# Optimization experiments

Measured on AMD Instinct MI355X. Metric: run time of the kernel, lower is better.

## Reference

```python
import jax, jax.numpy as jnp
import numpy as np

N = 100000

def _norm_edges(edge_index, n):
    # add self loops, compute symmetric GCN normalization
    loop = jnp.arange(n, dtype=edge_index.dtype)
    src = jnp.concatenate([edge_index[0], loop])
    dst = jnp.concatenate([edge_index[1], loop])
    deg = jax.ops.segment_sum(jnp.ones_like(dst, dtype=jnp.float32), dst, num_segments=n)
    dinv = jnp.where(deg > 0, deg ** -0.5, 0.0)
    norm = dinv[src] * dinv[dst]
    return src, dst, norm

def _gcn(x, W, b, src, dst, norm, n):
    h = x @ W  # [N, out]
    msg = h[src] * norm[:, None]
    return jax.ops.segment_sum(msg, dst, num_segments=n) + b

def setup_inputs() -> dict:
    key = jax.random.key(0)
    ks = jax.random.split(key, 20)
    E = 3200000
    d_in, d_out = 64, 64
    def w(k, i, o):
        return jax.random.normal(k, (i, o), dtype=jnp.float32) * (1.0 / np.sqrt(i))
    return {
        "x": jax.random.normal(ks[0], (N, d_in), dtype=jnp.float32),
        "t": jax.random.normal(ks[1], (N,), dtype=jnp.float32),
        "edge_index": jax.random.randint(ks[2], (2, E), 0, N, dtype=jnp.int64),
        "W1": w(ks[3], d_in + 1, 64), "b1": jnp.zeros((64,), jnp.float32),
        "W2": w(ks[4], 64, 128), "b2": jnp.zeros((128,), jnp.float32),
        "W3": w(ks[5], 128, 256), "b3": jnp.zeros((256,), jnp.float32),
        "W4": w(ks[6], 256, 128), "b4": jnp.zeros((128,), jnp.float32),
        "F1": w(ks[7], 128, 256), "c1": jnp.zeros((256,), jnp.float32),
        "F2": w(ks[8], 256, 128), "c2": jnp.zeros((128,), jnp.float32),
        "F3": w(ks[9], 128, d_out), "c3": jnp.zeros((d_out,), jnp.float32),
    }

def reference(x, t, edge_index, W1, b1, W2, b2, W3, b3, W4, b4, F1, c1, F2, c2, F3, c3):
    n = x.shape[0]
    src, dst, norm = _norm_edges(edge_index, n)
    h = jnp.concatenate([x, t[:, None]], axis=1)
    h = jax.nn.gelu(_gcn(h, W1, b1, src, dst, norm, n))
    h = jax.nn.gelu(_gcn(h, W2, b2, src, dst, norm, n))
    h = jax.nn.gelu(_gcn(h, W3, b3, src, dst, norm, n))
    h = jax.nn.gelu(_gcn(h, W4, b4, src, dst, norm, n))
    h = jax.nn.gelu(h @ F1 + c1)
    h = jax.nn.gelu(h @ F2 + c2)
    return h @ F3 + c3
```

## Files before the change

### kernel.cpp

```cpp
#include <hip/hip_runtime.h>

static constexpr int BLK = 256;

typedef double d2 __attribute__((ext_vector_type(2)));
typedef int    i4 __attribute__((ext_vector_type(4)));

__device__ __forceinline__ double gelu_d(double v){
  double u = 0.7978845608028654 * (v + 0.044715 * v * v * v);
  return 0.5 * v * (1.0 + tanh(u));
}

__global__ void zero_k(int* __restrict__ a, int n){
  int stride = gridDim.x * blockDim.x;
  for (int i = blockIdx.x*blockDim.x + threadIdx.x; i < n; i += stride) a[i] = 0;
}

__global__ void zeromax_k(unsigned long long* m){
  if (threadIdx.x == 0 && blockIdx.x == 0)
    for (int i = 0; i < 8; ++i) m[i] = 0ull;
}

__global__ void detect_k(const int* __restrict__ ei, int* __restrict__ flag){
  if (threadIdx.x == 0 && blockIdx.x == 0){
    int zeros = 0;
    for (int i = 0; i < 64; ++i) if (ei[2*i + 1] == 0) ++zeros;
    *flag = (zeros >= 48) ? 1 : 0;
  }
}

__global__ void count_k(const int* __restrict__ ei, int E, const int* __restrict__ flag,
                        int* __restrict__ cnt){
  int is64 = *flag;
  int stride = gridDim.x * blockDim.x;
  for (int e = blockIdx.x*blockDim.x + threadIdx.x; e < E; e += stride){
    int d = is64 ? ei[2*(E + e)] : ei[E + e];
    atomicAdd(&cnt[d], 1);
  }
}

__global__ void dinv_k(const int* __restrict__ cnt, double* __restrict__ dinv, int n){
  int i = blockIdx.x*blockDim.x + threadIdx.x;
  if (i < n){
    double deg = (double)(cnt[i] + 1);
    dinv[i] = 1.0 / sqrt(deg);
  }
}

__global__ __launch_bounds__(256)
void scanA_k(const int* __restrict__ cnt, int* __restrict__ partial, int n, int chunk){
  __shared__ int red[256];
  int b = blockIdx.x;
  int lo = b * chunk, hi = min(n, lo + chunk);
  int s = 0;
  for (int i = lo + threadIdx.x; i < hi; i += 256) s += cnt[i];
  red[threadIdx.x] = s; __syncthreads();
  for (int off = 128; off > 0; off >>= 1){
    if (threadIdx.x < off) red[threadIdx.x] += red[threadIdx.x + off];
    __syncthreads();
  }
  if (threadIdx.x == 0) partial[b] = red[0];
}

__global__ __launch_bounds__(256)
void scanB_k(int* __restrict__ partial, int nb){
  __shared__ int sd[256];
  int tid = threadIdx.x;
  int v = (tid < nb) ? partial[tid] : 0;
  sd[tid] = v; __syncthreads();
  for (int off = 1; off < 256; off <<= 1){
    int t = (tid >= off) ? sd[tid - off] : 0;
    __syncthreads();
    sd[tid] += t;
    __syncthreads();
  }
  if (tid < nb) partial[tid] = sd[tid] - v;
  if (tid == 255) partial[nb] = sd[255];
}

__global__ __launch_bounds__(256)
void scanC_k(const int* __restrict__ cnt, const int* __restrict__ partial,
             int* __restrict__ rp, int n, int chunk, int nb){
  __shared__ int sd[256];
  int b = blockIdx.x;
  int lo = b * chunk, hi = min(n, lo + chunk);
  int run = partial[b];
  for (int base = lo; base < hi; base += 256){
    int i = base + threadIdx.x;
    int v = (i < hi) ? cnt[i] : 0;
    sd[threadIdx.x] = v; __syncthreads();
    for (int off = 1; off < 256; off <<= 1){
      int t = (threadIdx.x >= off) ? sd[threadIdx.x - off] : 0;
      __syncthreads();
      sd[threadIdx.x] += t;
      __syncthreads();
    }
    if (i < hi) rp[i] = run + sd[threadIdx.x] - v;
    run += sd[255];
    __syncthreads();
  }
  if (b == 0 && threadIdx.x == 0) rp[n] = partial[nb];
}

__global__ void scatter_k(const int* __restrict__ ei, int E, const int* __restrict__ flag,
                          const int* __restrict__ rp, int* __restrict__ fill,
                          const double* __restrict__ dinv,
                          int* __restrict__ col, double* __restrict__ val){
  int is64 = *flag;
  int stride = gridDim.x * blockDim.x;
  for (int e = blockIdx.x*blockDim.x + threadIdx.x; e < E; e += stride){
    int s = is64 ? ei[2*e]       : ei[e];
    int d = is64 ? ei[2*(E + e)] : ei[E + e];
    int p = rp[d] + atomicAdd(&fill[d], 1);
    col[p] = s;
    if (val) val[p] = dinv[s];
  }
}

template<typename ST>
__global__ void concat_k(const float* __restrict__ x, const float* __restrict__ t,
                         ST* __restrict__ h0, int n){
  int total = n * 66;
  int stride = gridDim.x * blockDim.x;
  for (int idx = blockIdx.x*blockDim.x + threadIdx.x; idx < total; idx += stride){
    int row = idx / 66;
    int c = idx - row * 66;
    float v = (c < 64) ? x[row*64 + c] : (c == 64 ? t[row] : 0.0f);
    h0[idx] = (ST)v;
  }
}

template<typename ST>
__global__ __launch_bounds__(256, 4)
void gemm_k(const ST* __restrict__ A, int K, int lda,
            const float* __restrict__ W, int NOUT,
            const float* __restrict__ bias,
            ST* __restrict__ C, float* __restrict__ Cf,
            int n, int fuse)
{
  __shared__ __align__(16) double As[128][18];
  __shared__ __align__(16) double Ws[16][66];
  const int row0 = blockIdx.x * 128;
  const int col0 = blockIdx.y * 64;
  const int tid = threadIdx.x;
  const int tr = tid >> 4, tc = tid & 15;
  const int c0 = 2 * tc;
  double acc[8][4] = {};

  const int sar = tid >> 1;
  const int sak = (tid & 1) * 8;
  const int swr = tid >> 4;
  const int swc = (tid & 15) * 4;

  const int ktiles = (K + 15) / 16;

  double ga[8];
  float  gw[4];

  auto loadA = [&](int k0){
    int gr = row0 + sar;
    if constexpr (sizeof(ST) == 8){
      if (gr < n){
        const double* Ap = (const double*)A + (size_t)gr * lda + k0 + sak;
        #pragma unroll
        for (int g = 0; g < 4; ++g){
          d2 v = *(const d2*)(Ap + 2*g);
          ga[2*g] = v.x; ga[2*g+1] = v.y;
        }
      } else {
        #pragma unroll
        for (int u = 0; u < 8; ++u) ga[u] = 0.0;
      }
    } else {
      const ST* Ap = A + (size_t)gr * lda + k0 + sak;
      #pragma unroll
      for (int u = 0; u < 8; ++u){
        int kg = k0 + sak + u;
        ga[u] = (gr < n && kg < K) ? (double)Ap[u] : 0.0;
      }
    }
  };
  auto loadW = [&](int k0){
    int kg = k0 + swr;
    if (kg < K){
      const float* Wp = W + (size_t)kg * NOUT + col0 + swc;
      #pragma unroll
      for (int g = 0; g < 4; ++g) gw[g] = Wp[g];
    } else {
      #pragma unroll
      for (int g = 0; g < 4; ++g) gw[g] = 0.0f;
    }
  };

  loadA(0);
  loadW(0);

  for (int kt = 0; kt < ktiles; ++kt){
    #pragma unroll
    for (int g = 0; g < 4; ++g){
      d2 v; v.x = ga[2*g]; v.y = ga[2*g+1];
      *(d2*)&As[sar][sak + 2*g] = v;
    }
    {
      d2 v0; v0.x = (double)gw[0]; v0.y = (double)gw[1];
      d2 v1; v1.x = (double)gw[2]; v1.y = (double)gw[3];
      *(d2*)&Ws[swr][swc]     = v0;
      *(d2*)&Ws[swr][swc + 2] = v1;
    }
    __syncthreads();
    if (kt + 1 < ktiles){
      loadA((kt + 1) * 16);
      loadW((kt + 1) * 16);
    }
    #pragma unroll
    for (int kk = 0; kk < 16; kk += 2){
      d2 w0a = *(const d2*)&Ws[kk    ][c0];
      d2 w0b = *(const d2*)&Ws[kk    ][c0 + 32];
      d2 w1a = *(const d2*)&Ws[kk + 1][c0];
      d2 w1b = *(const d2*)&Ws[kk + 1][c0 + 32];
      #pragma unroll
      for (int i = 0; i < 8; ++i){
        d2 av = *(const d2*)&As[tr + 16*i][kk];
        acc[i][0] = fma(av.x, w0a.x, acc[i][0]);
        acc[i][1] = fma(av.x, w0a.y, acc[i][1]);
        acc[i][2] = fma(av.x, w0b.x, acc[i][2]);
        acc[i][3] = fma(av.x, w0b.y, acc[i][3]);
        acc[i][0] = fma(av.y, w1a.x, acc[i][0]);
        acc[i][1] = fma(av.y, w1a.y, acc[i][1]);
        acc[i][2] = fma(av.y, w1b.x, acc[i][2]);
        acc[i][3] = fma(av.y, w1b.y, acc[i][3]);
      }
    }
    __syncthreads();
  }
  #pragma unroll
  for (int i = 0; i < 8; ++i){
    int r = row0 + tr + 16*i;
    if (r >= n) continue;
    #pragma unroll
    for (int j = 0; j < 4; ++j){
      int c = col0 + ((j < 2) ? (c0 + j) : (c0 + 30 + j));
      double v = acc[i][j];
      if (fuse){ v += (double)bias[c]; if (fuse == 1) v = gelu_d(v); }
      if (fuse == 2) __builtin_nontemporal_store((float)v, &Cf[(size_t)r * NOUT + c]);
      else           __builtin_nontemporal_store((ST)v,   &C [(size_t)r * NOUT + c]);
    }
  }
}


__global__ void absmaxW_k(const float* __restrict__ W, int n, unsigned long long* __restrict__ out){
  double tmax = 0.0;
  int stride = gridDim.x * blockDim.x;
  for (int i = blockIdx.x*blockDim.x + threadIdx.x; i < n; i += stride)
    tmax = fmax(tmax, (double)fabsf(W[i]));
  #pragma unroll
  for (int off = 32; off > 0; off >>= 1)
    tmax = fmax(tmax, __shfl_xor(tmax, off));
  if ((threadIdx.x & 63) == 0)
    atomicMax(out, (unsigned long long)__double_as_longlong(tmax));
}

__global__ __launch_bounds__(256)
void absmaxD_k(const double* __restrict__ a, size_t L, unsigned long long* __restrict__ out){
  __shared__ double red[256];
  double tmax = 0.0;
  size_t stride = (size_t)gridDim.x * blockDim.x;
  for (size_t i = blockIdx.x*(size_t)blockDim.x + threadIdx.x; i < L; i += stride)
    tmax = fmax(tmax, fabs(a[i]));
  red[threadIdx.x] = tmax; __syncthreads();
  for (int off = 128; off > 0; off >>= 1){
    if (threadIdx.x < off) red[threadIdx.x] = fmax(red[threadIdx.x], red[threadIdx.x + off]);
    __syncthreads();
  }
  if (threadIdx.x == 0)
    atomicMax(out, (unsigned long long)__double_as_longlong(red[0]));
}

__global__ void quantW_k(const float* __restrict__ W, int K, int N,
                         const unsigned long long* __restrict__ maxw,
                         char* __restrict__ WqT){
  double wm = __longlong_as_double((long long)*maxw);
  int sw = (wm > 0.0) ? (36 - ilogb(wm)) : 0;
  double sc = ldexp(1.0, sw);
  int total = K * N;
  size_t NK = (size_t)N * K;
  int stride = gridDim.x * blockDim.x;
  for (int t = blockIdx.x*blockDim.x + threadIdx.x; t < total; t += stride){
    int k = t / N, nn = t - k * N;
    long long v = __double2ll_rn((double)W[t] * sc);
    #pragma unroll
    for (int p = 0; p < 5; ++p){
      int d = (int)((v + 128) & 255) - 128;
      WqT[(size_t)p * NK + (size_t)nn * K + k] = (char)d;
      v = (v - d) >> 8;
    }
  }
}

template<int K>
__global__ __launch_bounds__(512)
void ozaki_k(const double* __restrict__ A, const char* __restrict__ WqT,
             const unsigned long long* __restrict__ maxa,
             const unsigned long long* __restrict__ maxw,
             const float* __restrict__ bias,
             double* __restrict__ C, unsigned long long* __restrict__ amaxOut,
             int n, int NOUT, int fuse)
{
  constexpr int PAD = 16;
  constexpr int PP[22] = {0,0,0, 1,1,1,1, 2,2,2,2,2, 3,3,3,3,3, 4,4,4,4,4};
  constexpr int QQ[22] = {2,3,4, 1,2,3,4, 0,1,2,3,4, 0,1,2,3,4, 0,1,2,3,4};
  __shared__ __align__(16) char laq[5][16][K + PAD];
  __shared__ double red[8];
  const int tid  = threadIdx.x;
  const int lane = tid & 63;
  const int ct   = tid >> 6;
  const int l15  = lane & 15;
  const int lk   = lane >> 4;
  const int row0 = blockIdx.x * 16;
  const int col0g = blockIdx.y * 128;

  double am = __longlong_as_double((long long)*maxa);
  double wm = __longlong_as_double((long long)*maxw);
  int sa = (am > 0.0) ? (37 - ilogb(am)) : 0;
  int sw = (wm > 0.0) ? (36 - ilogb(wm)) : 0;
  double sc = ldexp(1.0, sa);

  {
    int r = tid >> 5;
    int gr = row0 + r; if (gr >= n) gr = n - 1;
    if constexpr (K == 256){
      int kq = (tid & 31) * 8;
      const double* Ap = A + (size_t)gr * K + kq;
      unsigned long long pack[5] = {0,0,0,0,0};
      #pragma unroll
      for (int u = 0; u < 8; ++u){
        long long v = __double2ll_rn(Ap[u] * sc);
        #pragma unroll
        for (int p = 0; p < 5; ++p){
          int d = (int)((v + 128) & 255) - 128;
          pack[p] |= (unsigned long long)(unsigned char)d << (8*u);
          v = (v - d) >> 8;
        }
      }
      #pragma unroll
      for (int p = 0; p < 5; ++p)
        *(unsigned long long*)&laq[p][r][kq] = pack[p];
    } else {
      int kq = (tid & 31) * 4;
      const double* Ap = A + (size_t)gr * K + kq;
      unsigned int pack[5] = {0,0,0,0,0};
      #pragma unroll
      for (int u = 0; u < 4; ++u){
        long long v = __double2ll_rn(Ap[u] * sc);
        #pragma unroll
        for (int p = 0; p < 5; ++p){
          int d = (int)((v + 128) & 255) - 128;
          pack[p] |= (unsigned int)(unsigned char)d << (8*u);
          v = (v - d) >> 8;
        }
      }
      #pragma unroll
      for (int p = 0; p < 5; ++p)
        *(unsigned int*)&laq[p][r][kq] = pack[p];
    }
  }
  __syncthreads();

  i4 acc[22];
  #pragma unroll
  for (int i = 0; i < 22; ++i){ i4 z = {0,0,0,0}; acc[i] = z; }

  const size_t NK = (size_t)NOUT * K;
  const char* wb = WqT + (size_t)(col0g + ct * 16 + l15) * K + lk * 16;
  #pragma unroll
  for (int ks = 0; ks < K / 64; ++ks){
    int k0 = ks * 64;
    i4 af[5], bf[5];
    #pragma unroll
    for (int p = 0; p < 5; ++p)
      af[p] = *(const i4*)&laq[p][l15][k0 + lk*16];
    #pragma unroll
    for (int q = 0; q < 5; ++q)
      bf[q] = *(const i4*)(wb + (size_t)q * NK + k0);
    #pragma unroll
    for (int i = 0; i < 22; ++i)
      acc[i] = __builtin_amdgcn_mfma_i32_16x16x64_i8(af[PP[i]], bf[QQ[i]], acc[i], 0, 0, 0);
  }

  double s = ldexp(1.0, -(sa + sw));
  double w8[9];
  #pragma unroll
  for (int e = 2; e <= 8; ++e) w8[e] = ldexp(s, 8 * e);
  double tmax = 0.0;
  #pragma unroll
  for (int m = 0; m < 4; ++m){
    int r = row0 + lk * 4 + m;
    int c = col0g + ct * 16 + l15;
    long long g[9] = {};
    #pragma unroll
    for (int i = 0; i < 22; ++i) g[PP[i] + QQ[i]] += acc[i][m];
    double sum = 0.0;
    #pragma unroll
    for (int e = 2; e <= 8; ++e) sum = fma((double)g[e], w8[e], sum);
    double v = sum;
    if (fuse) v = gelu_d(v + (double)bias[c]);
    if (r < n){
      __builtin_nontemporal_store(v, &C[(size_t)r * NOUT + c]);
      tmax = fmax(tmax, fabs(v));
    }
  }
  if (amaxOut){
    #pragma unroll
    for (int off = 32; off > 0; off >>= 1)
      tmax = fmax(tmax, __shfl_xor(tmax, off));
    if (lane == 0) red[ct] = tmax;
    __syncthreads();
    if (tid == 0){
      double mv = red[0];
      #pragma unroll
      for (int i = 1; i < 8; ++i) mv = fmax(mv, red[i]);
      atomicMax(amaxOut, (unsigned long long)__double_as_longlong(mv));
    }
  }
}

template<typename ST, int NC>
__global__ __launch_bounds__(256)
void agg_k(const ST* __restrict__ T, const int* __restrict__ rp,
           const int* __restrict__ col, const double* __restrict__ val,
           const double* __restrict__ dinv, const float* __restrict__ bias,
           ST* __restrict__ O, int n, int fuse)
{
  constexpr int DOUT = NC * 64;
  int w = (blockIdx.x * blockDim.x + threadIdx.x) >> 6;
  int lane = threadIdx.x & 63;
  if (w >= n) return;
  double dv = dinv[w];
  const ST* Ti = T + (size_t)w * DOUT;
  double acc[NC];
  #pragma unroll
  for (int c = 0; c < NC; ++c) acc[c] = dv * (double)Ti[lane + 64*c];
  int e  = rp[w];
  int e1 = rp[w + 1];
  if (val){
    for (; e + 4 <= e1; e += 4){
      int s0 = __builtin_nontemporal_load(&col[e]);
      int s1 = __builtin_nontemporal_load(&col[e+1]);
      int s2 = __builtin_nontemporal_load(&col[e+2]);
      int s3 = __builtin_nontemporal_load(&col[e+3]);
      double v0 = __builtin_nontemporal_load(&val[e]);
      double v1 = __builtin_nontemporal_load(&val[e+1]);
      double v2 = __builtin_nontemporal_load(&val[e+2]);
      double v3 = __builtin_nontemporal_load(&val[e+3]);
      const ST* T0 = T + (size_t)s0 * DOUT;
      const ST* T1 = T + (size_t)s1 * DOUT;
      const ST* T2 = T + (size_t)s2 * DOUT;
      const ST* T3 = T + (size_t)s3 * DOUT;
      double t0[NC], t1[NC], t2[NC], t3[NC];
      #pragma unroll
      for (int c = 0; c < NC; ++c){
        t0[c] = (double)T0[lane + 64*c];
        t1[c] = (double)T1[lane + 64*c];
        t2[c] = (double)T2[lane + 64*c];
        t3[c] = (double)T3[lane + 64*c];
      }
      #pragma unroll
      for (int c = 0; c < NC; ++c){
        acc[c] = fma(v0, t0[c], acc[c]);
        acc[c] = fma(v1, t1[c], acc[c]);
        acc[c] = fma(v2, t2[c], acc[c]);
        acc[c] = fma(v3, t3[c], acc[c]);
      }
    }
    for (; e < e1; ++e){
      int s = __builtin_nontemporal_load(&col[e]);
      double v = __builtin_nontemporal_load(&val[e]);
      const ST* Ts = T + (size_t)s * DOUT;
      #pragma unroll
      for (int c = 0; c < NC; ++c) acc[c] = fma(v, (double)Ts[lane + 64*c], acc[c]);
    }
  } else {
    for (; e < e1; ++e){
      int s = col[e];
      double v = dinv[s];
      const ST* Ts = T + (size_t)s * DOUT;
      #pragma unroll
      for (int c = 0; c < NC; ++c) acc[c] = fma(v, (double)Ts[lane + 64*c], acc[c]);
    }
  }
  ST* Oi = O + (size_t)w * DOUT;
  #pragma unroll
  for (int c = 0; c < NC; ++c){
    double v = dv * acc[c];
    if (fuse) v = gelu_d(v + (double)bias[lane + 64*c]);
    __builtin_nontemporal_store((ST)v, &Oi[lane + 64*c]);
  }
}

template<typename ST>
static void run_net(const float* x, const float* t,
                    const float* W1, const float* b1, const float* W2, const float* b2,
                    const float* W3, const float* b3, const float* W4, const float* b4,
                    const float* F1, const float* c1, const float* F2, const float* c2,
                    const float* F3, const float* c3,
                    ST* b256, ST* ba, ST* bb,
                    const int* rp, const int* col, const double* val, const double* dinv,
                    char* Wq3, char* Wq4, char* WqF1, char* WqF2,
                    unsigned long long* mx, bool ozk,
                    float* out, int N, hipStream_t stream)
{
  auto gemm = [&](const ST* A, int K, int lda, const float* W, int NOUT, const float* bias,
                  ST* C, float* Cf, int fuse){
    dim3 g((N + 127) / 128, NOUT / 64);
    gemm_k<ST><<<g, dim3(BLK), 0, stream>>>(A, K, lda, W, NOUT, bias, C, Cf, N, fuse);
  };
  int aggGrid = (N * 64 + BLK - 1) / BLK;
  auto agg64 = [&](const ST* T, const float* bias, ST* O, int fuse){
    agg_k<ST,1><<<dim3(aggGrid), dim3(BLK), 0, stream>>>(T, rp, col, val, dinv, bias, O, N, fuse);
  };
  auto agg128 = [&](const ST* T, const float* bias, ST* O, int fuse){
    agg_k<ST,2><<<dim3(aggGrid), dim3(BLK), 0, stream>>>(T, rp, col, val, dinv, bias, O, N, fuse);
  };

  concat_k<ST><<<dim3(1024), dim3(BLK), 0, stream>>>(x, t, ba, N);
  gemm(ba, 65, 66, W1, 64, nullptr, bb, nullptr, 0);
  agg64(bb, b1, ba, 1);
  agg64(ba, nullptr, bb, 0);
  gemm(bb, 64, 64, W2, 128, b2, ba, nullptr, 1);
  agg128(ba, nullptr, bb, 0);
  if (ozk){
    if constexpr (sizeof(ST) == 8){
      double* dbb = (double*)bb; double* db256 = (double*)b256; double* dba = (double*)ba;
      dim3 gK128((N + 15) / 16, 2), gK256((N + 15) / 16, 1);
      absmaxD_k<<<dim3(2048), dim3(256), 0, stream>>>(dbb, (size_t)N * 128, mx + 0);
      ozaki_k<128><<<gK128, dim3(512), 0, stream>>>(dbb, Wq3, mx + 0, mx + 1, b3,
                                                    db256, mx + 2, N, 256, 1);
      ozaki_k<256><<<gK256, dim3(512), 0, stream>>>(db256, Wq4, mx + 2, mx + 3, nullptr,
                                                    dba, nullptr, N, 128, 0);
      agg128(ba, b4, bb, 1);
      absmaxD_k<<<dim3(2048), dim3(256), 0, stream>>>(dbb, (size_t)N * 128, mx + 4);
      ozaki_k<128><<<gK128, dim3(512), 0, stream>>>(dbb, WqF1, mx + 4, mx + 5, c1,
                                                    db256, mx + 6, N, 256, 1);
      ozaki_k<256><<<gK256, dim3(512), 0, stream>>>(db256, WqF2, mx + 6, mx + 7, c2,
                                                    dba, nullptr, N, 128, 1);
    }
  } else {
    gemm(bb, 128, 128, W3, 256, b3, b256, nullptr, 1);
    gemm(b256, 256, 256, W4, 128, nullptr, ba, nullptr, 0);
    agg128(ba, b4, bb, 1);
    gemm(bb, 128, 128, F1, 256, c1, b256, nullptr, 1);
    gemm(b256, 256, 256, F2, 128, c2, ba, nullptr, 1);
  }
  gemm(ba, 128, 128, F3, 64, c3, nullptr, out, 2);
}

extern "C" void kernel_launch(void* const* d_in, const int* in_sizes, int n_in,
                              void* d_out, int out_size, void* d_ws, size_t ws_size,
                              hipStream_t stream)
{
  const float* x  = (const float*)d_in[0];
  const float* t  = (const float*)d_in[1];
  const int*   ei = (const int*)d_in[2];
  const float* W1 = (const float*)d_in[3];  const float* b1 = (const float*)d_in[4];
  const float* W2 = (const float*)d_in[5];  const float* b2 = (const float*)d_in[6];
  const float* W3 = (const float*)d_in[7];  const float* b3 = (const float*)d_in[8];
  const float* W4 = (const float*)d_in[9];  const float* b4 = (const float*)d_in[10];
  const float* F1 = (const float*)d_in[11]; const float* c1 = (const float*)d_in[12];
  const float* F2 = (const float*)d_in[13]; const float* c2 = (const float*)d_in[14];
  const float* F3 = (const float*)d_in[15]; const float* c3 = (const float*)d_in[16];
  float* out = (float*)d_out;
  int N = in_sizes[0] / 64;
  int E = in_sizes[2] / 2;

  char* p = (char*)d_ws;
  auto alloc = [&](size_t b){ char* r = p; p += (b + 255) & ~(size_t)255; return (void*)r; };
  int*    flag    = (int*)alloc(4);
  int*    cnt     = (int*)alloc((size_t)N * 4);
  int*    fill    = (int*)alloc((size_t)N * 4);
  int*    rp      = (int*)alloc((size_t)(N + 1) * 4);
  int*    partial = (int*)alloc((size_t)257 * 4);
  int*    col     = (int*)alloc((size_t)E * 4);
  double* dinv    = (double*)alloc((size_t)N * 8);
  size_t base = (size_t)(p - (char*)d_ws);

  size_t slackB   = 1024;
  size_t actB     = (size_t)N * 512 * sizeof(double) + 3 * slackB;
  size_t actB32   = (size_t)N * 512 * sizeof(float) + 3 * slackB;
  size_t valBytes = ((size_t)E * 8 + 255) & ~(size_t)255;
  size_t wqB      = 5 * 128 * 256;
  size_t wqTotal  = 256 + 4 * wqB + 8 * 256;

  bool ozk    = ws_size >= base + wqTotal + valBytes + actB;
  bool f64val = ozk || ws_size >= base + valBytes + actB;
  bool f64ok  = f64val || ws_size >= base + actB;
  bool f32val = ws_size >= base + valBytes + actB32;
  bool f32ok  = f32val || ws_size >= base + actB32;
  if (!f64ok && !f32ok) return;

  unsigned long long* mx = nullptr;
  char *Wq3 = nullptr, *Wq4 = nullptr, *WqF1 = nullptr, *WqF2 = nullptr;
  if (ozk){
    mx   = (unsigned long long*)alloc(256);
    Wq3  = (char*)alloc(wqB);
    Wq4  = (char*)alloc(wqB);
    WqF1 = (char*)alloc(wqB);
    WqF2 = (char*)alloc(wqB);
  }

  double* val = nullptr;
  if (f64ok ? f64val : f32val) val = (double*)alloc((size_t)E * 8);

  int nb = 256;
  int chunk = (N + nb - 1) / nb;
  zero_k<<<dim3(256), dim3(BLK), 0, stream>>>(cnt, N);
  zero_k<<<dim3(256), dim3(BLK), 0, stream>>>(fill, N);
  detect_k<<<1, 64, 0, stream>>>(ei, flag);
  count_k<<<dim3(4096), dim3(BLK), 0, stream>>>(ei, E, flag, cnt);
  dinv_k<<<dim3((N + BLK - 1) / BLK), dim3(BLK), 0, stream>>>(cnt, dinv, N);
  scanA_k<<<dim3(nb), dim3(256), 0, stream>>>(cnt, partial, N, chunk);
  scanB_k<<<dim3(1), dim3(256), 0, stream>>>(partial, nb);
  scanC_k<<<dim3(nb), dim3(256), 0, stream>>>(cnt, partial, rp, N, chunk, nb);
  scatter_k<<<dim3(4096), dim3(BLK), 0, stream>>>(ei, E, flag, rp, fill, dinv, col, val);

  if (ozk){
    zeromax_k<<<1, 64, 0, stream>>>(mx);
    absmaxW_k<<<dim3(32), dim3(BLK), 0, stream>>>(W3, 128 * 256, mx + 1);
    quantW_k<<<dim3(128), dim3(BLK), 0, stream>>>(W3, 128, 256, mx + 1, Wq3);
    absmaxW_k<<<dim3(32), dim3(BLK), 0, stream>>>(W4, 256 * 128, mx + 3);
    quantW_k<<<dim3(128), dim3(BLK), 0, stream>>>(W4, 256, 128, mx + 3, Wq4);
    absmaxW_k<<<dim3(32), dim3(BLK), 0, stream>>>(F1, 128 * 256, mx + 5);
    quantW_k<<<dim3(128), dim3(BLK), 0, stream>>>(F1, 128, 256, mx + 5, WqF1);
    absmaxW_k<<<dim3(32), dim3(BLK), 0, stream>>>(F2, 256 * 128, mx + 7);
    quantW_k<<<dim3(128), dim3(BLK), 0, stream>>>(F2, 256, 128, mx + 7, WqF2);
  }

  if (f64ok){
    double* b256 = (double*)alloc((size_t)N * 256 * 8 + slackB);
    double* ba   = (double*)alloc((size_t)N * 128 * 8 + slackB);
    double* bb   = (double*)alloc((size_t)N * 128 * 8 + slackB);
    run_net<double>(x, t, W1, b1, W2, b2, W3, b3, W4, b4, F1, c1, F2, c2, F3, c3,
                    b256, ba, bb, rp, col, val, dinv,
                    Wq3, Wq4, WqF1, WqF2, mx, ozk, out, N, stream);
  } else {
    float* b256 = (float*)alloc((size_t)N * 256 * 4 + slackB);
    float* ba   = (float*)alloc((size_t)N * 128 * 4 + slackB);
    float* bb   = (float*)alloc((size_t)N * 128 * 4 + slackB);
    run_net<float>(x, t, W1, b1, W2, b2, W3, b3, W4, b4, F1, c1, F2, c2, F3, c3,
                   b256, ba, bb, rp, col, val, dinv,
                   nullptr, nullptr, nullptr, nullptr, nullptr, false, out, N, stream);
  }
}
```

Before: 2.543 ms.

## Drop per-edge weight array and reuse scratch buffers for quantized weights

Removes the precomputed per-edge double val array. The aggregation kernel now gathers dinv[src] directly, which cuts scatter writes and per-edge streaming reads at the cost of an extra random gather per edge. Weight quantization is moved inline before each Ozaki GEMM, and the cnt and fill buffers are reused as scratch for the quantized weights and absmax values. This lowers workspace needs so the f64/Ozaki path can be enabled with a smaller workspace, at the risk of aliasing bugs if those buffers are too small or still in use.

```diff
diff --git a/kernel.cpp b/kernel.cpp
--- a/kernel.cpp
+++ b/kernel.cpp
@@ -103,8 +103,7 @@
 
 __global__ void scatter_k(const int* __restrict__ ei, int E, const int* __restrict__ flag,
                           const int* __restrict__ rp, int* __restrict__ fill,
-                          const double* __restrict__ dinv,
-                          int* __restrict__ col, double* __restrict__ val){
+                          int* __restrict__ col){
   int is64 = *flag;
   int stride = gridDim.x * blockDim.x;
   for (int e = blockIdx.x*blockDim.x + threadIdx.x; e < E; e += stride){
@@ -112,7 +111,6 @@
     int d = is64 ? ei[2*(E + e)] : ei[E + e];
     int p = rp[d] + atomicAdd(&fill[d], 1);
     col[p] = s;
-    if (val) val[p] = dinv[s];
   }
 }
 
@@ -427,9 +425,8 @@
 template<typename ST, int NC>
 __global__ __launch_bounds__(256)
 void agg_k(const ST* __restrict__ T, const int* __restrict__ rp,
-           const int* __restrict__ col, const double* __restrict__ val,
-           const double* __restrict__ dinv, const float* __restrict__ bias,
-           ST* __restrict__ O, int n, int fuse)
+           const int* __restrict__ col, const double* __restrict__ dinv,
+           const float* __restrict__ bias, ST* __restrict__ O, int n, int fuse)
 {
   constexpr int DOUT = NC * 64;
   int w = (blockIdx.x * blockDim.x + threadIdx.x) >> 6;
@@ -442,51 +439,41 @@
   for (int c = 0; c < NC; ++c) acc[c] = dv * (double)Ti[lane + 64*c];
   int e  = rp[w];
   int e1 = rp[w + 1];
-  if (val){
-    for (; e + 4 <= e1; e += 4){
-      int s0 = __builtin_nontemporal_load(&col[e]);
-      int s1 = __builtin_nontemporal_load(&col[e+1]);
-      int s2 = __builtin_nontemporal_load(&col[e+2]);
-      int s3 = __builtin_nontemporal_load(&col[e+3]);
-      double v0 = __builtin_nontemporal_load(&val[e]);
-      double v1 = __builtin_nontemporal_load(&val[e+1]);
-      double v2 = __builtin_nontemporal_load(&val[e+2]);
-      double v3 = __builtin_nontemporal_load(&val[e+3]);
-      const ST* T0 = T + (size_t)s0 * DOUT;
-      const ST* T1 = T + (size_t)s1 * DOUT;
-      const ST* T2 = T + (size_t)s2 * DOUT;
-      const ST* T3 = T + (size_t)s3 * DOUT;
-      double t0[NC], t1[NC], t2[NC], t3[NC];
-      #pragma unroll
-      for (int c = 0; c < NC; ++c){
-        t0[c] = (double)T0[lane + 64*c];
-        t1[c] = (double)T1[lane + 64*c];
-        t2[c] = (double)T2[lane + 64*c];
-        t3[c] = (double)T3[lane + 64*c];
-      }
-      #pragma unroll
-      for (int c = 0; c < NC; ++c){
-        acc[c] = fma(v0, t0[c], acc[c]);
-        acc[c] = fma(v1, t1[c], acc[c]);
-        acc[c] = fma(v2, t2[c], acc[c]);
-        acc[c] = fma(v3, t3[c], acc[c]);
-      }
-    }
-    for (; e < e1; ++e){
-      int s = __builtin_nontemporal_load(&col[e]);
-      double v = __builtin_nontemporal_load(&val[e]);
-      const ST* Ts = T + (size_t)s * DOUT;
-      #pragma unroll
-      for (int c = 0; c < NC; ++c) acc[c] = fma(v, (double)Ts[lane + 64*c], acc[c]);
-    }
-  } else {
-    for (; e < e1; ++e){
-      int s = col[e];
-      double v = dinv[s];
-      const ST* Ts = T + (size_t)s * DOUT;
-      #pragma unroll
-      for (int c = 0; c < NC; ++c) acc[c] = fma(v, (double)Ts[lane + 64*c], acc[c]);
-    }
+  for (; e + 4 <= e1; e += 4){
+    int s0 = __builtin_nontemporal_load(&col[e]);
+    int s1 = __builtin_nontemporal_load(&col[e+1]);
+    int s2 = __builtin_nontemporal_load(&col[e+2]);
+    int s3 = __builtin_nontemporal_load(&col[e+3]);
+    double v0 = dinv[s0];
+    double v1 = dinv[s1];
+    double v2 = dinv[s2];
+    double v3 = dinv[s3];
+    const ST* T0 = T + (size_t)s0 * DOUT;
+    const ST* T1 = T + (size_t)s1 * DOUT;
+    const ST* T2 = T + (size_t)s2 * DOUT;
+    const ST* T3 = T + (size_t)s3 * DOUT;
+    double t0[NC], t1[NC], t2[NC], t3[NC];
+    #pragma unroll
+    for (int c = 0; c < NC; ++c){
+      t0[c] = (double)T0[lane + 64*c];
+      t1[c] = (double)T1[lane + 64*c];
+      t2[c] = (double)T2[lane + 64*c];
+      t3[c] = (double)T3[lane + 64*c];
+    }
+    #pragma unroll
+    for (int c = 0; c < NC; ++c){
+      acc[c] = fma(v0, t0[c], acc[c]);
+      acc[c] = fma(v1, t1[c], acc[c]);
+      acc[c] = fma(v2, t2[c], acc[c]);
+      acc[c] = fma(v3, t3[c], acc[c]);
+    }
+  }
+  for (; e < e1; ++e){
+    int s = __builtin_nontemporal_load(&col[e]);
+    double v = dinv[s];
+    const ST* Ts = T + (size_t)s * DOUT;
+    #pragma unroll
+    for (int c = 0; c < NC; ++c) acc[c] = fma(v, (double)Ts[lane + 64*c], acc[c]);
   }
   ST* Oi = O + (size_t)w * DOUT;
   #pragma unroll
@@ -504,9 +491,8 @@
                     const float* F1, const float* c1, const float* F2, const float* c2,
                     const float* F3, const float* c3,
                     ST* b256, ST* ba, ST* bb,
-                    const int* rp, const int* col, const double* val, const double* dinv,
-                    char* Wq3, char* Wq4, char* WqF1, char* WqF2,
-                    unsigned long long* mx, bool ozk,
+                    const int* rp, const int* col, const double* dinv,
+                    char* Wq, unsigned long long* mx, bool ozk,
                     float* out, int N, hipStream_t stream)
 {
   auto gemm = [&](const ST* A, int K, int lda, const float* W, int NOUT, const float* bias,
@@ -516,10 +502,10 @@
   };
   int aggGrid = (N * 64 + BLK - 1) / BLK;
   auto agg64 = [&](const ST* T, const float* bias, ST* O, int fuse){
-    agg_k<ST,1><<<dim3(aggGrid), dim3(BLK), 0, stream>>>(T, rp, col, val, dinv, bias, O, N, fuse);
+    agg_k<ST,1><<<dim3(aggGrid), dim3(BLK), 0, stream>>>(T, rp, col, dinv, bias, O, N, fuse);
   };
   auto agg128 = [&](const ST* T, const float* bias, ST* O, int fuse){
-    agg_k<ST,2><<<dim3(aggGrid), dim3(BLK), 0, stream>>>(T, rp, col, val, dinv, bias, O, N, fuse);
+    agg_k<ST,2><<<dim3(aggGrid), dim3(BLK), 0, stream>>>(T, rp, col, dinv, bias, O, N, fuse);
   };
 
   concat_k<ST><<<dim3(1024), dim3(BLK), 0, stream>>>(x, t, ba, N);
@@ -532,16 +518,25 @@
     if constexpr (sizeof(ST) == 8){
       double* dbb = (double*)bb; double* db256 = (double*)b256; double* dba = (double*)ba;
       dim3 gK128((N + 15) / 16, 2), gK256((N + 15) / 16, 1);
+      zeromax_k<<<1, 64, 0, stream>>>(mx);
       absmaxD_k<<<dim3(2048), dim3(256), 0, stream>>>(dbb, (size_t)N * 128, mx + 0);
-      ozaki_k<128><<<gK128, dim3(512), 0, stream>>>(dbb, Wq3, mx + 0, mx + 1, b3,
+      absmaxW_k<<<dim3(32), dim3(BLK), 0, stream>>>(W3, 128 * 256, mx + 1);
+      quantW_k<<<dim3(128), dim3(BLK), 0, stream>>>(W3, 128, 256, mx + 1, Wq);
+      ozaki_k<128><<<gK128, dim3(512), 0, stream>>>(dbb, Wq, mx + 0, mx + 1, b3,
                                                     db256, mx + 2, N, 256, 1);
-      ozaki_k<256><<<gK256, dim3(512), 0, stream>>>(db256, Wq4, mx + 2, mx + 3, nullptr,
+      absmaxW_k<<<dim3(32), dim3(BLK), 0, stream>>>(W4, 256 * 128, mx + 3);
+      quantW_k<<<dim3(128), dim3(BLK), 0, stream>>>(W4, 256, 128, mx + 3, Wq);
+      ozaki_k<256><<<gK256, dim3(512), 0, stream>>>(db256, Wq, mx + 2, mx + 3, nullptr,
                                                     dba, nullptr, N, 128, 0);
       agg128(ba, b4, bb, 1);
       absmaxD_k<<<dim3(2048), dim3(256), 0, stream>>>(dbb, (size_t)N * 128, mx + 4);
-      ozaki_k<128><<<gK128, dim3(512), 0, stream>>>(dbb, WqF1, mx + 4, mx + 5, c1,
+      absmaxW_k<<<dim3(32), dim3(BLK), 0, stream>>>(F1, 128 * 256, mx + 5);
+      quantW_k<<<dim3(128), dim3(BLK), 0, stream>>>(F1, 128, 256, mx + 5, Wq);
+      ozaki_k<128><<<gK128, dim3(512), 0, stream>>>(dbb, Wq, mx + 4, mx + 5, c1,
                                                     db256, mx + 6, N, 256, 1);
-      ozaki_k<256><<<gK256, dim3(512), 0, stream>>>(db256, WqF2, mx + 6, mx + 7, c2,
+      absmaxW_k<<<dim3(32), dim3(BLK), 0, stream>>>(F2, 256 * 128, mx + 7);
+      quantW_k<<<dim3(128), dim3(BLK), 0, stream>>>(F2, 256, 128, mx + 7, Wq);
+      ozaki_k<256><<<gK256, dim3(512), 0, stream>>>(db256, Wq, mx + 6, mx + 7, c2,
                                                     dba, nullptr, N, 128, 1);
     }
   } else {
@@ -583,35 +578,17 @@
   double* dinv    = (double*)alloc((size_t)N * 8);
   size_t base = (size_t)(p - (char*)d_ws);
 
-  size_t slackB   = 1024;
-  size_t actB     = (size_t)N * 512 * sizeof(double) + 3 * slackB;
-  size_t actB32   = (size_t)N * 512 * sizeof(float) + 3 * slackB;
-  size_t valBytes = ((size_t)E * 8 + 255) & ~(size_t)255;
-  size_t wqB      = 5 * 128 * 256;
-  size_t wqTotal  = 256 + 4 * wqB + 8 * 256;
-
-  bool ozk    = ws_size >= base + wqTotal + valBytes + actB;
-  bool f64val = ozk || ws_size >= base + valBytes + actB;
-  bool f64ok  = f64val || ws_size >= base + actB;
-  bool f32val = ws_size >= base + valBytes + actB32;
-  bool f32ok  = f32val || ws_size >= base + actB32;
-  if (!f64ok && !f32ok) return;
-
-  unsigned long long* mx = nullptr;
-  char *Wq3 = nullptr, *Wq4 = nullptr, *WqF1 = nullptr, *WqF2 = nullptr;
-  if (ozk){
-    mx   = (unsigned long long*)alloc(256);
-    Wq3  = (char*)alloc(wqB);
-    Wq4  = (char*)alloc(wqB);
-    WqF1 = (char*)alloc(wqB);
-    WqF2 = (char*)alloc(wqB);
-  }
-
-  double* val = nullptr;
-  if (f64ok ? f64val : f32val) val = (double*)alloc((size_t)E * 8);
+  size_t slackB = 1024;
+  size_t actB   = (size_t)N * 512 * 8 + 3 * slackB;
+  size_t actB32 = (size_t)N * 512 * 4 + 3 * slackB;
+
+  bool f64base = ws_size >= base + actB;
+  bool f32base = ws_size >= base + actB32;
+  if (!f64base && !f32base) return;
 
   int nb = 256;
   int chunk = (N + nb - 1) / nb;
+
   zero_k<<<dim3(256), dim3(BLK), 0, stream>>>(cnt, N);
   zero_k<<<dim3(256), dim3(BLK), 0, stream>>>(fill, N);
   detect_k<<<1, 64, 0, stream>>>(ei, flag);
@@ -620,33 +597,23 @@
   scanA_k<<<dim3(nb), dim3(256), 0, stream>>>(cnt, partial, N, chunk);
   scanB_k<<<dim3(1), dim3(256), 0, stream>>>(partial, nb);
   scanC_k<<<dim3(nb), dim3(256), 0, stream>>>(cnt, partial, rp, N, chunk, nb);
-  scatter_k<<<dim3(4096), dim3(BLK), 0, stream>>>(ei, E, flag, rp, fill, dinv, col, val);
-
-  if (ozk){
-    zeromax_k<<<1, 64, 0, stream>>>(mx);
-    absmaxW_k<<<dim3(32), dim3(BLK), 0, stream>>>(W3, 128 * 256, mx + 1);
-    quantW_k<<<dim3(128), dim3(BLK), 0, stream>>>(W3, 128, 256, mx + 1, Wq3);
-    absmaxW_k<<<dim3(32), dim3(BLK), 0, stream>>>(W4, 256 * 128, mx + 3);
-    quantW_k<<<dim3(128), dim3(BLK), 0, stream>>>(W4, 256, 128, mx + 3, Wq4);
-    absmaxW_k<<<dim3(32), dim3(BLK), 0, stream>>>(F1, 128 * 256, mx + 5);
-    quantW_k<<<dim3(128), dim3(BLK), 0, stream>>>(F1, 128, 256, mx + 5, WqF1);
-    absmaxW_k<<<dim3(32), dim3(BLK), 0, stream>>>(F2, 256 * 128, mx + 7);
-    quantW_k<<<dim3(128), dim3(BLK), 0, stream>>>(F2, 256, 128, mx + 7, WqF2);
-  }
-
-  if (f64ok){
+  scatter_k<<<dim3(4096), dim3(BLK), 0, stream>>>(ei, E, flag, rp, fill, col);
+  char* Wq = (char*)cnt;
+  unsigned long long* mx = (unsigned long long*)fill;
+
+  if (f64base){
     double* b256 = (double*)alloc((size_t)N * 256 * 8 + slackB);
     double* ba   = (double*)alloc((size_t)N * 128 * 8 + slackB);
     double* bb   = (double*)alloc((size_t)N * 128 * 8 + slackB);
     run_net<double>(x, t, W1, b1, W2, b2, W3, b3, W4, b4, F1, c1, F2, c2, F3, c3,
-                    b256, ba, bb, rp, col, val, dinv,
-                    Wq3, Wq4, WqF1, WqF2, mx, ozk, out, N, stream);
+                    b256, ba, bb, rp, col, dinv,
+                    Wq, mx, true, out, N, stream);
   } else {
     float* b256 = (float*)alloc((size_t)N * 256 * 4 + slackB);
     float* ba   = (float*)alloc((size_t)N * 128 * 4 + slackB);
     float* bb   = (float*)alloc((size_t)N * 128 * 4 + slackB);
     run_net<float>(x, t, W1, b1, W2, b2, W3, b3, W4, b4, F1, c1, F2, c2, F3, c3,
-                   b256, ba, bb, rp, col, val, dinv,
-                   nullptr, nullptr, nullptr, nullptr, nullptr, false, out, N, stream);
-  }
-}
+                   b256, ba, bb, rp, col, dinv,
+                   nullptr, nullptr, false, out, N, stream);
+  }
+}
```

After: 2.532 ms. No clear change (-0.4%).
